# Kernel optimization log

Hardware: AMD Instinct MI355X
Metric: run time of the kernel (lower is better)

Reference implementation:

```python
import jax, jax.numpy as jnp
import numpy as np

N = 100000
E = 1600000
IN_FEATS = 512
N_HIDDEN = 128
N_CLASSES = 40


def setup_inputs() -> dict:
    key = jax.random.key(0)
    k1, k2, k3, k4, k5, k6, k7 = jax.random.split(key, 7)
    inputs = jax.random.normal(k1, (N, IN_FEATS), dtype=jnp.float32)
    edge_index = jax.random.randint(k2, (2, E), 0, N, dtype=jnp.int64)
    edge_attr = jax.random.uniform(k3, (E,), dtype=jnp.float32)
    # GCNConv params (Glorot-ish scaling)
    W1 = jax.random.normal(k4, (IN_FEATS, N_HIDDEN), dtype=jnp.float32) / np.sqrt(IN_FEATS)
    b1 = jnp.zeros((N_HIDDEN,), dtype=jnp.float32)
    W2 = jax.random.normal(k5, (N_HIDDEN, N_CLASSES), dtype=jnp.float32) / np.sqrt(N_HIDDEN)
    b2 = jnp.zeros((N_CLASSES,), dtype=jnp.float32)
    return {"inputs": inputs, "edge_index": edge_index, "edge_attr": edge_attr,
            "W1": W1, "b1": b1, "W2": W2, "b2": b2}


def gcn_conv(x, W, b, src, dst, edge_weight):
    """GCNConv with normalize=False: linear transform, then edge-weighted
    scatter-sum from src to dst, then bias."""
    m = x @ W                                   # [N, F_out]
    msgs = m[src] * edge_weight[:, None]        # gather + weight, [E, F_out]
    agg = jax.ops.segment_sum(msgs, dst, num_segments=x.shape[0])  # scatter-add
    return agg + b


def reference(inputs, edge_index, edge_attr, W1, b1, W2, b2):
    src, dst = edge_index[0], edge_index[1]
    h = jax.nn.relu(gcn_conv(inputs, W1, b1, src, dst, edge_attr))
    # F.dropout with training=False (eval mode) is identity -> deterministic baseline
    preds = gcn_conv(h, W2, b2, src, dst, edge_attr)
    return jax.nn.log_softmax(preds, axis=1)
```

## Files before the change

kernel.cpp:

```cpp
#include <hip/hip_runtime.h>
#include <hip/hip_bf16.h>
#include <cstdint>

#define N_NODES 100000
#define N_EDGES 1600000
#define F_IN    512
#define F_HID   128
#define F_OUT   40
#define F_OUT_PAD 48

#define BSH    8
#define NB     391
#define BEPT   8
#define BCHUNK 4096
#define GB     391
#define CONVB  140
#define FCAP   6144
#define DBINS  64

typedef short v8s __attribute__((ext_vector_type(8)));
typedef float v4f __attribute__((ext_vector_type(4)));

__device__ __forceinline__ short f2bf(float f) {
    unsigned u = __float_as_uint(f);
    u += 0x7fffu + ((u >> 16) & 1u);
    return (short)(u >> 16);
}

__device__ __forceinline__ float bflo(unsigned u) { return __uint_as_float(u << 16); }
__device__ __forceinline__ float bfhi(unsigned u) { return __uint_as_float(u & 0xffff0000u); }

__device__ __forceinline__ v8s pack8(float4 a, float4 b) {
    v8s r;
    r[0] = f2bf(a.x); r[1] = f2bf(a.y); r[2] = f2bf(a.z); r[3] = f2bf(a.w);
    r[4] = f2bf(b.x); r[5] = f2bf(b.y); r[6] = f2bf(b.z); r[7] = f2bf(b.w);
    return r;
}

__device__ __forceinline__ void gload16(const void* g, void* l) {
    __builtin_amdgcn_global_load_lds(
        (const __attribute__((address_space(1))) void*)g,
        (__attribute__((address_space(3))) void*)l, 16, 0, 0);
}


__global__ __launch_bounds__(512) void k_bhist(const int* __restrict__ dst,
                                               int* __restrict__ bcnt,
                                               const float* __restrict__ W1,
                                               short* __restrict__ WT1,
                                               const float* __restrict__ W2,
                                               short* __restrict__ WT2) {
    if (blockIdx.x >= GB) {
        int i = (blockIdx.x - GB) * 512 + threadIdx.x;
        if (i < F_IN * F_HID) {
            int n = i >> 9, k = i & 511;
            WT1[i] = f2bf(W1[k * F_HID + n]);
        } else {
            int j = i - F_IN * F_HID;
            if (j < F_OUT_PAD * F_HID) {
                int n = j >> 7, k = j & 127;
                WT2[j] = (n < F_OUT) ? f2bf(W2[k * F_OUT + n]) : (short)0;
            }
        }
        return;
    }
    __shared__ int lh[512];
    int tid = threadIdx.x;
    lh[tid] = 0;
    __syncthreads();
    long e0 = (long)blockIdx.x * BCHUNK;
#pragma unroll
    for (int i = 0; i < BEPT; i++) {
        long e = e0 + tid + i * 512;
        if (e < N_EDGES) atomicAdd(&lh[dst[e] >> BSH], 1);
    }
    __syncthreads();
    if (tid < NB && lh[tid]) atomicAdd(&bcnt[tid], lh[tid]);
}

__global__ __launch_bounds__(512) void k_bscan(const int* __restrict__ bcnt,
                                               int* __restrict__ bbase,
                                               int* __restrict__ bcur) {
    __shared__ int sm[512];
    int tid = threadIdx.x;
    int v = (tid < NB) ? bcnt[tid] : 0;
    sm[tid] = v;
    __syncthreads();
    for (int off = 1; off < 512; off <<= 1) {
        int t = (tid >= off) ? sm[tid - off] : 0;
        __syncthreads();
        sm[tid] += t;
        __syncthreads();
    }
    if (tid < NB) {
        int ex = sm[tid] - v;
        bbase[tid] = ex;
        bcur[tid] = ex;
    }
    if (tid == 511) bbase[NB] = sm[511];
}

__global__ __launch_bounds__(512) void k_bscatter(const int* __restrict__ src,
                                                  const int* __restrict__ dst,
                                                  const float* __restrict__ w,
                                                  int* __restrict__ bcur,
                                                  int2* __restrict__ tmp) {
    __shared__ int cntA[512];
    __shared__ int ofsA[512];
    __shared__ int lcur[512];
    __shared__ int gb[512];
    __shared__ __align__(16) int2 recBuf[BCHUNK];
    __shared__ unsigned short bkt[BCHUNK];
    int tid = threadIdx.x;
    long e0 = (long)blockIdx.x * BCHUNK;
    cntA[tid] = 0;
    __syncthreads();

    int dloc[BEPT];
#pragma unroll
    for (int i = 0; i < BEPT; i++) {
        long e = e0 + tid + i * 512;
        int d = (e < N_EDGES) ? dst[e] : -1;
        dloc[i] = d;
        if (d >= 0) atomicAdd(&cntA[d >> BSH], 1);
    }
    __syncthreads();

    int v = cntA[tid];
    ofsA[tid] = v;
    __syncthreads();
    for (int off = 1; off < 512; off <<= 1) {
        int t = (tid >= off) ? ofsA[tid - off] : 0;
        __syncthreads();
        ofsA[tid] += t;
        __syncthreads();
    }
    int excl = ofsA[tid] - v;
    ofsA[tid] = excl;
    lcur[tid] = excl;
    if (tid < NB && v > 0) gb[tid] = atomicAdd(&bcur[tid], v);
    __syncthreads();

#pragma unroll
    for (int i = 0; i < BEPT; i++) {
        int d = dloc[i];
        if (d >= 0) {
            long e = e0 + tid + i * 512;
            int j = d >> BSH;
            int slot = atomicAdd(&lcur[j], 1);
            recBuf[slot] = make_int2(src[e] | ((d & 255) << 17), __float_as_int(w[e]));
            bkt[slot] = (unsigned short)j;
        }
    }
    __syncthreads();

    long rem = N_EDGES - e0;
    int total = (rem < BCHUNK) ? (int)rem : BCHUNK;
    for (int s = tid; s < total; s += 512) {
        int j = bkt[s];
        tmp[gb[j] + (s - ofsA[j])] = recBuf[s];
    }
}

__global__ __launch_bounds__(256) void k_fine(const int2* __restrict__ tmp,
                                              const int* __restrict__ bbase,
                                              int2* __restrict__ rec,
                                              int* __restrict__ rowptr,
                                              int* __restrict__ deg,
                                              int* __restrict__ dcnt) {
    __shared__ int hist[256];
    __shared__ int ofs[256];
    __shared__ int cur[256];
    __shared__ int dh[DBINS];
    __shared__ __align__(16) int2 recOut[FCAP];
    int tid = threadIdx.x, b = blockIdx.x;
    int base = bbase[b];
    int cnt = bbase[b + 1] - base;

    hist[tid] = 0;
    if (tid < DBINS) dh[tid] = 0;
    __syncthreads();
    for (int i = tid; i < cnt; i += 256) {
        unsigned u = (unsigned)tmp[base + i].x;
        atomicAdd(&hist[u >> 17], 1);
    }
    __syncthreads();

    int v = hist[tid];
    ofs[tid] = v;
    __syncthreads();
    for (int off = 1; off < 256; off <<= 1) {
        int t = (tid >= off) ? ofs[tid - off] : 0;
        __syncthreads();
        ofs[tid] += t;
        __syncthreads();
    }
    int excl = ofs[tid] - v;
    ofs[tid] = excl;
    cur[tid] = excl;
    int node = (b << BSH) + tid;
    if (node < N_NODES) {
        rowptr[node] = base + excl;
        deg[node] = v;
        atomicAdd(&dh[v < DBINS ? v : DBINS - 1], 1);
    }
    __syncthreads();
    if (tid < DBINS && dh[tid]) atomicAdd(&dcnt[tid], dh[tid]);

    if (cnt <= FCAP) {
        for (int i = tid; i < cnt; i += 256) {
            int2 r = tmp[base + i];
            unsigned u = (unsigned)r.x;
            int slot = atomicAdd(&cur[u >> 17], 1);
            recOut[slot] = make_int2((int)(u & 0x1FFFFu), r.y);
        }
        __syncthreads();
        for (int i = tid; i < cnt; i += 256) rec[base + i] = recOut[i];
    } else {
        for (int i = tid; i < cnt; i += 256) {
            int2 r = tmp[base + i];
            unsigned u = (unsigned)r.x;
            int slot = atomicAdd(&cur[u >> 17], 1);
            rec[base + slot] = make_int2((int)(u & 0x1FFFFu), r.y);
        }
    }
}

__global__ __launch_bounds__(DBINS) void k_dscan(const int* __restrict__ dcnt,
                                                 int* __restrict__ dcur) {
    __shared__ int sm[DBINS];
    int tid = threadIdx.x;
    int v = dcnt[tid];
    sm[tid] = v;
    __syncthreads();
    for (int off = 1; off < DBINS; off <<= 1) {
        int t = (tid >= off) ? sm[tid - off] : 0;
        __syncthreads();
        sm[tid] += t;
        __syncthreads();
    }
    dcur[tid] = sm[tid] - v;
}

__global__ __launch_bounds__(256) void k_dscatter(const int* __restrict__ rowptr,
                                                  const int* __restrict__ deg,
                                                  int* __restrict__ dcur,
                                                  int4* __restrict__ ninfo) {
    __shared__ int lh[DBINS];
    __shared__ int gbase[DBINS];
    int tid = threadIdx.x;
    if (tid < DBINS) lh[tid] = 0;
    __syncthreads();
    int node = blockIdx.x * 256 + tid;
    int d = 0, lpos = 0, st = 0, ct = 0;
    bool valid = node < N_NODES;
    if (valid) {
        st = rowptr[node];
        ct = deg[node];
        d = ct < DBINS ? ct : DBINS - 1;
        lpos = atomicAdd(&lh[d], 1);
    }
    __syncthreads();
    if (tid < DBINS && lh[tid]) gbase[tid] = atomicAdd(&dcur[tid], lh[tid]);
    __syncthreads();
    if (valid) ninfo[gbase[d] + lpos] = make_int4(node, st, ct, 0);
}


__global__ __launch_bounds__(256) void k_gemm1(const float* __restrict__ x,
                                               const short* __restrict__ WT1,
                                               unsigned short* __restrict__ m1b) {
    __shared__ __align__(16) float aBuf[2][64 * 32];
    __shared__ __align__(16) short bBuf[2][128 * 32];
    int tid = threadIdx.x, w = tid >> 6, lane = tid & 63;
    int quad = lane >> 4, l16 = lane & 15;
    long rowBase = (long)blockIdx.x * 64;

    int ar = lane >> 3, ac = lane & 7;
    int br = lane >> 2, bc = lane & 3;

    v4f acc[8];
#pragma unroll
    for (int t = 0; t < 8; t++) acc[t] = (v4f){0.f, 0.f, 0.f, 0.f};

    auto stage = [&](int kc, int buf) {
#pragma unroll
        for (int i = 0; i < 2; i++) {
            int rl = w * 16 + i * 8 + ar;
            long rg = rowBase + rl;
            if (rg > N_NODES - 1) rg = N_NODES - 1;
            const float* gp = x + rg * F_IN + kc * 32 + ((ac ^ (rl & 7)) << 2);
            gload16(gp, &aBuf[buf][(w * 16 + i * 8) * 32]);
        }
#pragma unroll
        for (int i = 0; i < 2; i++) {
            int n = w * 32 + i * 16 + br;
            const short* gp = WT1 + n * F_IN + kc * 32 + ((bc ^ ((n >> 1) & 3)) << 3);
            gload16(gp, &bBuf[buf][(w * 32 + i * 16) * 32]);
        }
    };

    stage(0, 0);
#pragma unroll
    for (int kc = 0; kc < 16; kc++) {
        __syncthreads();
        int buf = kc & 1;
        if (kc < 15) stage(kc + 1, buf ^ 1);
        int arow = w * 16 + l16;
        int p0 = (2 * quad) ^ (l16 & 7);
        float4 av0 = *(const float4*)&aBuf[buf][arow * 32 + p0 * 4];
        float4 av1 = *(const float4*)&aBuf[buf][arow * 32 + (p0 ^ 1) * 4];
        v8s af = pack8(av0, av1);
#pragma unroll
        for (int t = 0; t < 8; t++) {
            int n = t * 16 + l16;
            int p = quad ^ ((n >> 1) & 3);
            v8s bf = *(const v8s*)&bBuf[buf][n * 32 + p * 8];
            acc[t] = __builtin_amdgcn_mfma_f32_16x16x32_bf16(af, bf, acc[t], 0, 0, 0);
        }
    }

#pragma unroll
    for (int t = 0; t < 8; t++)
#pragma unroll
        for (int r = 0; r < 4; r++) {
            long row = rowBase + w * 16 + quad * 4 + r;
            if (row < N_NODES)
                m1b[row * F_HID + t * 16 + l16] = (unsigned short)f2bf(acc[t][r]);
        }
}


__global__ void k_agg1(const int2* __restrict__ rec, const int4* __restrict__ ninfo,
                       const uint4* __restrict__ m1v, const float* __restrict__ b1,
                       uint4* __restrict__ h4) {
    int gid = blockIdx.x * 4 + (threadIdx.x >> 6);
    int lane = threadIdx.x & 63;
    if (gid >= N_NODES) return;
    int4 ni = ninfo[gid];
    int node = ni.x, start = ni.y, cnt = ni.z;
    int q = lane >> 4, l16 = lane & 15;

    float a0 = 0.f, a1 = 0.f, a2 = 0.f, a3 = 0.f;
    float a4 = 0.f, a5 = 0.f, a6 = 0.f, a7 = 0.f;
    float c0 = 0.f, c1 = 0.f, c2 = 0.f, c3 = 0.f;
    float c4 = 0.f, c5 = 0.f, c6 = 0.f, c7 = 0.f;

    int nmain = cnt >> 3;
    int eb = start + q;
    for (int k = 0; k < nmain; k++) {
        int e = eb + (k << 3);
        int2 r0 = rec[e];
        int2 r1 = rec[e + 4];
        uint4 g0 = m1v[(long)r0.x * 16 + l16];
        uint4 g1 = m1v[(long)r1.x * 16 + l16];
        float w0 = __int_as_float(r0.y), w1 = __int_as_float(r1.y);
        a0 = fmaf(w0, bflo(g0.x), a0); a1 = fmaf(w0, bfhi(g0.x), a1);
        a2 = fmaf(w0, bflo(g0.y), a2); a3 = fmaf(w0, bfhi(g0.y), a3);
        a4 = fmaf(w0, bflo(g0.z), a4); a5 = fmaf(w0, bfhi(g0.z), a5);
        a6 = fmaf(w0, bflo(g0.w), a6); a7 = fmaf(w0, bfhi(g0.w), a7);
        c0 = fmaf(w1, bflo(g1.x), c0); c1 = fmaf(w1, bfhi(g1.x), c1);
        c2 = fmaf(w1, bflo(g1.y), c2); c3 = fmaf(w1, bfhi(g1.y), c3);
        c4 = fmaf(w1, bflo(g1.z), c4); c5 = fmaf(w1, bfhi(g1.z), c5);
        c6 = fmaf(w1, bflo(g1.w), c6); c7 = fmaf(w1, bfhi(g1.w), c7);
    }
    for (int e = start + (nmain << 3) + q; e < start + cnt; e += 4) {
        int2 r = rec[e];
        uint4 g = m1v[(long)r.x * 16 + l16];
        float w = __int_as_float(r.y);
        a0 = fmaf(w, bflo(g.x), a0); a1 = fmaf(w, bfhi(g.x), a1);
        a2 = fmaf(w, bflo(g.y), a2); a3 = fmaf(w, bfhi(g.y), a3);
        a4 = fmaf(w, bflo(g.z), a4); a5 = fmaf(w, bfhi(g.z), a5);
        a6 = fmaf(w, bflo(g.w), a6); a7 = fmaf(w, bfhi(g.w), a7);
    }
    a0 += c0; a1 += c1; a2 += c2; a3 += c3;
    a4 += c4; a5 += c5; a6 += c6; a7 += c7;
    a0 += __shfl_xor(a0, 16); a0 += __shfl_xor(a0, 32);
    a1 += __shfl_xor(a1, 16); a1 += __shfl_xor(a1, 32);
    a2 += __shfl_xor(a2, 16); a2 += __shfl_xor(a2, 32);
    a3 += __shfl_xor(a3, 16); a3 += __shfl_xor(a3, 32);
    a4 += __shfl_xor(a4, 16); a4 += __shfl_xor(a4, 32);
    a5 += __shfl_xor(a5, 16); a5 += __shfl_xor(a5, 32);
    a6 += __shfl_xor(a6, 16); a6 += __shfl_xor(a6, 32);
    a7 += __shfl_xor(a7, 16); a7 += __shfl_xor(a7, 32);
    if (q == 0) {
        const float4* b4 = (const float4*)b1;
        float4 bv0 = b4[2 * l16], bv1 = b4[2 * l16 + 1];
        a0 = fmaxf(a0 + bv0.x, 0.f); a1 = fmaxf(a1 + bv0.y, 0.f);
        a2 = fmaxf(a2 + bv0.z, 0.f); a3 = fmaxf(a3 + bv0.w, 0.f);
        a4 = fmaxf(a4 + bv1.x, 0.f); a5 = fmaxf(a5 + bv1.y, 0.f);
        a6 = fmaxf(a6 + bv1.z, 0.f); a7 = fmaxf(a7 + bv1.w, 0.f);
        uint4 o;
        o.x = (unsigned)(unsigned short)f2bf(a0) | ((unsigned)(unsigned short)f2bf(a1) << 16);
        o.y = (unsigned)(unsigned short)f2bf(a2) | ((unsigned)(unsigned short)f2bf(a3) << 16);
        o.z = (unsigned)(unsigned short)f2bf(a4) | ((unsigned)(unsigned short)f2bf(a5) << 16);
        o.w = (unsigned)(unsigned short)f2bf(a6) | ((unsigned)(unsigned short)f2bf(a7) << 16);
        h4[(long)node * 16 + l16] = o;
    }
}


__global__ __launch_bounds__(256) void k_gemm2(const unsigned short* __restrict__ h,
                                               const short* __restrict__ WT2,
                                               unsigned short* __restrict__ m2b) {
    int wave = threadIdx.x >> 6, lane = threadIdx.x & 63;
    int quad = lane >> 4, l16 = lane & 15;
    long rowBase = ((long)blockIdx.x * 4 + wave) * 16;
    if (rowBase >= N_NODES) return;

    v4f acc[3];
#pragma unroll
    for (int t = 0; t < 3; t++) acc[t] = (v4f){0.f, 0.f, 0.f, 0.f};

    const short* arow = (const short*)h + (rowBase + l16) * (long)F_HID + quad * 8;
    const short* brow = WT2 + l16 * F_HID + quad * 8;
#pragma unroll
    for (int k0 = 0; k0 < F_HID; k0 += 32) {
        v8s af = *reinterpret_cast<const v8s*>(arow + k0);
#pragma unroll
        for (int t = 0; t < 3; t++) {
            v8s bf = *reinterpret_cast<const v8s*>(brow + t * 16 * F_HID + k0);
            acc[t] = __builtin_amdgcn_mfma_f32_16x16x32_bf16(af, bf, acc[t], 0, 0, 0);
        }
    }
#pragma unroll
    for (int r = 0; r < 4; r++) {
        long row = rowBase + quad * 4 + r;
#pragma unroll
        for (int t = 0; t < 3; t++)
            m2b[row * 64 + t * 16 + l16] = (unsigned short)f2bf(acc[t][r]);
        m2b[row * 64 + 48 + l16] = 0;
    }
}


__global__ void k_agg2(const int2* __restrict__ rec, const int4* __restrict__ ninfo,
                       const uint4* __restrict__ m2v, const float* __restrict__ b2,
                       float* __restrict__ out) {
    int gid = blockIdx.x * 4 + (threadIdx.x >> 6);
    int lane = threadIdx.x & 63;
    if (gid >= N_NODES) return;
    int4 ni = ninfo[gid];
    int node = ni.x, start = ni.y, cnt = ni.z;
    int oc = lane >> 3, l8 = lane & 7;

    float a0 = 0.f, a1 = 0.f, a2 = 0.f, a3 = 0.f;
    float a4 = 0.f, a5 = 0.f, a6 = 0.f, a7 = 0.f;

    int nmain = cnt >> 3;
    int eb = start + oc;
    for (int k = 0; k < nmain; k++) {
        int2 r = rec[eb + (k << 3)];
        uint4 g = m2v[(long)r.x * 8 + l8];
        float w = __int_as_float(r.y);
        a0 = fmaf(w, bflo(g.x), a0); a1 = fmaf(w, bfhi(g.x), a1);
        a2 = fmaf(w, bflo(g.y), a2); a3 = fmaf(w, bfhi(g.y), a3);
        a4 = fmaf(w, bflo(g.z), a4); a5 = fmaf(w, bfhi(g.z), a5);
        a6 = fmaf(w, bflo(g.w), a6); a7 = fmaf(w, bfhi(g.w), a7);
    }
    {
        int e = start + (nmain << 3) + oc;
        if (e < start + cnt) {
            int2 r = rec[e];
            uint4 g = m2v[(long)r.x * 8 + l8];
            float w = __int_as_float(r.y);
            a0 = fmaf(w, bflo(g.x), a0); a1 = fmaf(w, bfhi(g.x), a1);
            a2 = fmaf(w, bflo(g.y), a2); a3 = fmaf(w, bfhi(g.y), a3);
            a4 = fmaf(w, bflo(g.z), a4); a5 = fmaf(w, bfhi(g.z), a5);
            a6 = fmaf(w, bflo(g.w), a6); a7 = fmaf(w, bfhi(g.w), a7);
        }
    }
#pragma unroll
    for (int off = 8; off < 64; off <<= 1) {
        a0 += __shfl_xor(a0, off); a1 += __shfl_xor(a1, off);
        a2 += __shfl_xor(a2, off); a3 += __shfl_xor(a3, off);
        a4 += __shfl_xor(a4, off); a5 += __shfl_xor(a5, off);
        a6 += __shfl_xor(a6, off); a7 += __shfl_xor(a7, off);
    }

    const float NEG = -3.4e38f;
    float v0 = NEG, v1 = NEG, v2 = NEG, v3 = NEG;
    float v4 = NEG, v5 = NEG, v6 = NEG, v7 = NEG;
    if (l8 < 5) {
        const float4* b4 = (const float4*)b2;
        float4 bv0 = b4[2 * l8], bv1 = b4[2 * l8 + 1];
        v0 = a0 + bv0.x; v1 = a1 + bv0.y; v2 = a2 + bv0.z; v3 = a3 + bv0.w;
        v4 = a4 + bv1.x; v5 = a5 + bv1.y; v6 = a6 + bv1.z; v7 = a7 + bv1.w;
    }
    float m = fmaxf(fmaxf(fmaxf(v0, v1), fmaxf(v2, v3)),
                    fmaxf(fmaxf(v4, v5), fmaxf(v6, v7)));
#pragma unroll
    for (int off = 1; off < 8; off <<= 1) m = fmaxf(m, __shfl_xor(m, off));
    float s = 0.f;
    if (l8 < 5)
        s = __expf(v0 - m) + __expf(v1 - m) + __expf(v2 - m) + __expf(v3 - m) +
            __expf(v4 - m) + __expf(v5 - m) + __expf(v6 - m) + __expf(v7 - m);
#pragma unroll
    for (int off = 1; off < 8; off <<= 1) s += __shfl_xor(s, off);
    if (oc == 0 && l8 < 5) {
        float ls = m + __logf(s);
        float4* op = (float4*)(out + (long)node * F_OUT);
        float4 o0, o1;
        o0.x = v0 - ls; o0.y = v1 - ls; o0.z = v2 - ls; o0.w = v3 - ls;
        o1.x = v4 - ls; o1.y = v5 - ls; o1.z = v6 - ls; o1.w = v7 - ls;
        op[2 * l8] = o0;
        op[2 * l8 + 1] = o1;
    }
}


extern "C" void kernel_launch(void* const* d_in, const int* in_sizes, int n_in,
                              void* d_out, int out_size, void* d_ws, size_t ws_size,
                              hipStream_t stream) {
    const float* x  = (const float*)d_in[0];
    const int* ei   = (const int*)d_in[1];
    const int* src  = ei;
    const int* dst  = ei + N_EDGES;
    const float* ew = (const float*)d_in[2];
    const float* W1 = (const float*)d_in[3];
    const float* b1 = (const float*)d_in[4];
    const float* W2 = (const float*)d_in[5];
    const float* b2 = (const float*)d_in[6];
    float* out = (float*)d_out;

    char* ws = (char*)d_ws;
    size_t off = 0;
    auto alloc = [&](size_t bytes) {
        void* p = ws + off;
        off += (bytes + 255) & ~(size_t)255;
        return p;
    };
    unsigned short* m1b  = (unsigned short*)alloc((size_t)N_NODES * F_HID * 2);
    unsigned int*   h    = (unsigned int*)alloc((size_t)N_NODES * F_HID * 2);
    unsigned short* m2b  = (unsigned short*)alloc((size_t)N_NODES * 64 * 2);
    int2*           rec  = (int2*)alloc((size_t)N_EDGES * 8);
    int*          rowptr = (int*)alloc((size_t)N_NODES * 4);
    int*          deg    = (int*)alloc((size_t)N_NODES * 4);
    int4*         ninfo  = (int4*)alloc((size_t)N_NODES * 16);
    int*          ctrl   = (int*)alloc(1024 * 4);
    int*          bBase  = (int*)alloc(512 * 4);
    int*          bCur   = (int*)alloc(512 * 4);
    short*        WT1    = (short*)alloc((size_t)F_HID * F_IN * 2);
    short*        WT2    = (short*)alloc((size_t)F_OUT_PAD * F_HID * 2);

    int* bCnt = ctrl;
    int* dcnt = ctrl + 512;
    int* dcur = ctrl + 576;

    int2* tmp = (int2*)m2b;

    hipMemsetAsync(ctrl, 0, 576 * 4, stream);

    k_bhist<<<GB + CONVB, 512, 0, stream>>>(dst, bCnt, W1, WT1, W2, WT2);
    k_bscan<<<1, 512, 0, stream>>>(bCnt, bBase, bCur);
    k_bscatter<<<GB, 512, 0, stream>>>(src, dst, ew, bCur, tmp);
    k_fine<<<NB, 256, 0, stream>>>(tmp, bBase, rec, rowptr, deg, dcnt);
    k_dscan<<<1, DBINS, 0, stream>>>(dcnt, dcur);
    k_dscatter<<<(N_NODES + 255) / 256, 256, 0, stream>>>(rowptr, deg, dcur, ninfo);

    k_gemm1<<<(N_NODES + 63) / 64, 256, 0, stream>>>(x, WT1, m1b);
    k_agg1<<<(N_NODES + 3) / 4, 256, 0, stream>>>(rec, ninfo, (const uint4*)m1b,
                                                  b1, (uint4*)h);
    k_gemm2<<<(N_NODES + 63) / 64, 256, 0, stream>>>((const unsigned short*)h, WT2, m2b);
    k_agg2<<<(N_NODES + 3) / 4, 256, 0, stream>>>(rec, ninfo, (const uint4*)m2b,
                                                  b2, out);
}
```

Measured before the change: 502.9 us.

## Fuse layer-1 aggregation with second GEMM and drop degree-sorted node ordering

Removes the degree-bucketing pipeline (histogram, scan and scatter kernels plus ninfo) and iterates nodes in natural order using rowptr/deg directly. Layer-1 aggregation now processes 16 consecutive nodes per wave, stages the bf16 hidden rows in swizzled LDS, and applies the W2 MFMA in-register, so the hidden matrix h never goes to global memory and k_gemm2 is eliminated. The edge loops are unrolled 4-way in the first layer and 2-way in the second. In exchange, removing degree sorting can cause load imbalance across waves, and each wave handles its 16 nodes serially.

Measured after the change: 491.0 us. 2.4% less time.

```diff
diff --git a/kernel.cpp b/kernel.cpp
--- a/kernel.cpp
+++ b/kernel.cpp
@@ -16,7 +16,6 @@
 #define GB     391
 #define CONVB  140
 #define FCAP   6144
-#define DBINS  64
 
 typedef short v8s __attribute__((ext_vector_type(8)));
 typedef float v4f __attribute__((ext_vector_type(4)));
@@ -166,19 +165,16 @@
                                               const int* __restrict__ bbase,
                                               int2* __restrict__ rec,
                                               int* __restrict__ rowptr,
-                                              int* __restrict__ deg,
-                                              int* __restrict__ dcnt) {
+                                              int* __restrict__ deg) {
     __shared__ int hist[256];
     __shared__ int ofs[256];
     __shared__ int cur[256];
-    __shared__ int dh[DBINS];
     __shared__ __align__(16) int2 recOut[FCAP];
     int tid = threadIdx.x, b = blockIdx.x;
     int base = bbase[b];
     int cnt = bbase[b + 1] - base;
 
     hist[tid] = 0;
-    if (tid < DBINS) dh[tid] = 0;
     __syncthreads();
     for (int i = tid; i < cnt; i += 256) {
         unsigned u = (unsigned)tmp[base + i].x;
@@ -202,10 +198,8 @@
     if (node < N_NODES) {
         rowptr[node] = base + excl;
         deg[node] = v;
-        atomicAdd(&dh[v < DBINS ? v : DBINS - 1], 1);
-    }
-    __syncthreads();
-    if (tid < DBINS && dh[tid]) atomicAdd(&dcnt[tid], dh[tid]);
+    }
+    __syncthreads();
 
     if (cnt <= FCAP) {
         for (int i = tid; i < cnt; i += 256) {
@@ -224,46 +218,6 @@
             rec[base + slot] = make_int2((int)(u & 0x1FFFFu), r.y);
         }
     }
-}
-
-__global__ __launch_bounds__(DBINS) void k_dscan(const int* __restrict__ dcnt,
-                                                 int* __restrict__ dcur) {
-    __shared__ int sm[DBINS];
-    int tid = threadIdx.x;
-    int v = dcnt[tid];
-    sm[tid] = v;
-    __syncthreads();
-    for (int off = 1; off < DBINS; off <<= 1) {
-        int t = (tid >= off) ? sm[tid - off] : 0;
-        __syncthreads();
-        sm[tid] += t;
-        __syncthreads();
-    }
-    dcur[tid] = sm[tid] - v;
-}
-
-__global__ __launch_bounds__(256) void k_dscatter(const int* __restrict__ rowptr,
-                                                  const int* __restrict__ deg,
-                                                  int* __restrict__ dcur,
-                                                  int4* __restrict__ ninfo) {
-    __shared__ int lh[DBINS];
-    __shared__ int gbase[DBINS];
-    int tid = threadIdx.x;
-    if (tid < DBINS) lh[tid] = 0;
-    __syncthreads();
-    int node = blockIdx.x * 256 + tid;
-    int d = 0, lpos = 0, st = 0, ct = 0;
-    bool valid = node < N_NODES;
-    if (valid) {
-        st = rowptr[node];
-        ct = deg[node];
-        d = ct < DBINS ? ct : DBINS - 1;
-        lpos = atomicAdd(&lh[d], 1);
-    }
-    __syncthreads();
-    if (tid < DBINS && lh[tid]) gbase[tid] = atomicAdd(&dcur[tid], lh[tid]);
-    __syncthreads();
-    if (valid) ninfo[gbase[d] + lpos] = make_int4(node, st, ct, 0);
 }
 
 
@@ -331,144 +285,182 @@
 }
 
 
-__global__ void k_agg1(const int2* __restrict__ rec, const int4* __restrict__ ninfo,
-                       const uint4* __restrict__ m1v, const float* __restrict__ b1,
-                       uint4* __restrict__ h4) {
-    int gid = blockIdx.x * 4 + (threadIdx.x >> 6);
+__global__ __launch_bounds__(256) void k_ag(const int2* __restrict__ rec,
+                                            const int* __restrict__ rowptr,
+                                            const int* __restrict__ deg,
+                                            const uint4* __restrict__ m1v,
+                                            const float* __restrict__ b1,
+                                            const short* __restrict__ WT2,
+                                            unsigned short* __restrict__ m2b) {
+    __shared__ uint4 ht[4][16][16];
+    int tid = threadIdx.x, w = tid >> 6, lane = tid & 63;
+    int q = lane >> 4, l16 = lane & 15;
+    int gBase = (blockIdx.x * 4 + w) * 16;
+
+    int idx = gBase + l16;
+    int rp = 0, dg = 0;
+    if (idx < N_NODES) { rp = rowptr[idx]; dg = deg[idx]; }
+    const float4* b4 = (const float4*)b1;
+    float4 bv0 = b4[2 * l16], bv1 = b4[2 * l16 + 1];
+
+    for (int i = 0; i < 16; i++) {
+        int start = __shfl(rp, i);
+        int cnt = __shfl(dg, i);
+        float a0 = 0.f, a1 = 0.f, a2 = 0.f, a3 = 0.f;
+        float a4 = 0.f, a5 = 0.f, a6 = 0.f, a7 = 0.f;
+        int e = start + q;
+        int n16 = cnt >> 4;
+        for (int k = 0; k < n16; k++) {
+            int2 r0 = rec[e];
+            int2 r1 = rec[e + 4];
+            int2 r2 = rec[e + 8];
+            int2 r3 = rec[e + 12];
+            uint4 g0 = m1v[(long)r0.x * 16 + l16];
+            uint4 g1 = m1v[(long)r1.x * 16 + l16];
+            uint4 g2 = m1v[(long)r2.x * 16 + l16];
+            uint4 g3 = m1v[(long)r3.x * 16 + l16];
+            float w0 = __int_as_float(r0.y), w1 = __int_as_float(r1.y);
+            float w2 = __int_as_float(r2.y), w3 = __int_as_float(r3.y);
+            a0 = fmaf(w0, bflo(g0.x), a0); a1 = fmaf(w0, bfhi(g0.x), a1);
+            a2 = fmaf(w0, bflo(g0.y), a2); a3 = fmaf(w0, bfhi(g0.y), a3);
+            a4 = fmaf(w0, bflo(g0.z), a4); a5 = fmaf(w0, bfhi(g0.z), a5);
+            a6 = fmaf(w0, bflo(g0.w), a6); a7 = fmaf(w0, bfhi(g0.w), a7);
+            a0 = fmaf(w1, bflo(g1.x), a0); a1 = fmaf(w1, bfhi(g1.x), a1);
+            a2 = fmaf(w1, bflo(g1.y), a2); a3 = fmaf(w1, bfhi(g1.y), a3);
+            a4 = fmaf(w1, bflo(g1.z), a4); a5 = fmaf(w1, bfhi(g1.z), a5);
+            a6 = fmaf(w1, bflo(g1.w), a6); a7 = fmaf(w1, bfhi(g1.w), a7);
+            a0 = fmaf(w2, bflo(g2.x), a0); a1 = fmaf(w2, bfhi(g2.x), a1);
+            a2 = fmaf(w2, bflo(g2.y), a2); a3 = fmaf(w2, bfhi(g2.y), a3);
+            a4 = fmaf(w2, bflo(g2.z), a4); a5 = fmaf(w2, bfhi(g2.z), a5);
+            a6 = fmaf(w2, bflo(g2.w), a6); a7 = fmaf(w2, bfhi(g2.w), a7);
+            a0 = fmaf(w3, bflo(g3.x), a0); a1 = fmaf(w3, bfhi(g3.x), a1);
+            a2 = fmaf(w3, bflo(g3.y), a2); a3 = fmaf(w3, bfhi(g3.y), a3);
+            a4 = fmaf(w3, bflo(g3.z), a4); a5 = fmaf(w3, bfhi(g3.z), a5);
+            a6 = fmaf(w3, bflo(g3.w), a6); a7 = fmaf(w3, bfhi(g3.w), a7);
+            e += 16;
+        }
+        if (cnt & 8) {
+            int2 r0 = rec[e];
+            int2 r1 = rec[e + 4];
+            uint4 g0 = m1v[(long)r0.x * 16 + l16];
+            uint4 g1 = m1v[(long)r1.x * 16 + l16];
+            float w0 = __int_as_float(r0.y), w1 = __int_as_float(r1.y);
+            a0 = fmaf(w0, bflo(g0.x), a0); a1 = fmaf(w0, bfhi(g0.x), a1);
+            a2 = fmaf(w0, bflo(g0.y), a2); a3 = fmaf(w0, bfhi(g0.y), a3);
+            a4 = fmaf(w0, bflo(g0.z), a4); a5 = fmaf(w0, bfhi(g0.z), a5);
+            a6 = fmaf(w0, bflo(g0.w), a6); a7 = fmaf(w0, bfhi(g0.w), a7);
+            a0 = fmaf(w1, bflo(g1.x), a0); a1 = fmaf(w1, bfhi(g1.x), a1);
+            a2 = fmaf(w1, bflo(g1.y), a2); a3 = fmaf(w1, bfhi(g1.y), a3);
+            a4 = fmaf(w1, bflo(g1.z), a4); a5 = fmaf(w1, bfhi(g1.z), a5);
+            a6 = fmaf(w1, bflo(g1.w), a6); a7 = fmaf(w1, bfhi(g1.w), a7);
+            e += 8;
+        }
+        for (int t = e; t < start + cnt; t += 4) {
+            int2 r = rec[t];
+            uint4 g = m1v[(long)r.x * 16 + l16];
+            float ww = __int_as_float(r.y);
+            a0 = fmaf(ww, bflo(g.x), a0); a1 = fmaf(ww, bfhi(g.x), a1);
+            a2 = fmaf(ww, bflo(g.y), a2); a3 = fmaf(ww, bfhi(g.y), a3);
+            a4 = fmaf(ww, bflo(g.z), a4); a5 = fmaf(ww, bfhi(g.z), a5);
+            a6 = fmaf(ww, bflo(g.w), a6); a7 = fmaf(ww, bfhi(g.w), a7);
+        }
+        a0 += __shfl_xor(a0, 16); a0 += __shfl_xor(a0, 32);
+        a1 += __shfl_xor(a1, 16); a1 += __shfl_xor(a1, 32);
+        a2 += __shfl_xor(a2, 16); a2 += __shfl_xor(a2, 32);
+        a3 += __shfl_xor(a3, 16); a3 += __shfl_xor(a3, 32);
+        a4 += __shfl_xor(a4, 16); a4 += __shfl_xor(a4, 32);
+        a5 += __shfl_xor(a5, 16); a5 += __shfl_xor(a5, 32);
+        a6 += __shfl_xor(a6, 16); a6 += __shfl_xor(a6, 32);
+        a7 += __shfl_xor(a7, 16); a7 += __shfl_xor(a7, 32);
+        if (q == 0) {
+            a0 = fmaxf(a0 + bv0.x, 0.f); a1 = fmaxf(a1 + bv0.y, 0.f);
+            a2 = fmaxf(a2 + bv0.z, 0.f); a3 = fmaxf(a3 + bv0.w, 0.f);
+            a4 = fmaxf(a4 + bv1.x, 0.f); a5 = fmaxf(a5 + bv1.y, 0.f);
+            a6 = fmaxf(a6 + bv1.z, 0.f); a7 = fmaxf(a7 + bv1.w, 0.f);
+            uint4 o;
+            o.x = (unsigned)(unsigned short)f2bf(a0) | ((unsigned)(unsigned short)f2bf(a1) << 16);
+            o.y = (unsigned)(unsigned short)f2bf(a2) | ((unsigned)(unsigned short)f2bf(a3) << 16);
+            o.z = (unsigned)(unsigned short)f2bf(a4) | ((unsigned)(unsigned short)f2bf(a5) << 16);
+            o.w = (unsigned)(unsigned short)f2bf(a6) | ((unsigned)(unsigned short)f2bf(a7) << 16);
+            ht[w][i][l16 ^ (i & 7)] = o;
+        }
+    }
+
+    v4f acc[3];
+#pragma unroll
+    for (int t = 0; t < 3; t++) acc[t] = (v4f){0.f, 0.f, 0.f, 0.f};
+#pragma unroll
+    for (int kk = 0; kk < 4; kk++) {
+        uint4 av = ht[w][l16][(kk * 4 + q) ^ (l16 & 7)];
+        v8s af = *reinterpret_cast<const v8s*>(&av);
+        const short* brow = WT2 + l16 * F_HID + q * 8 + kk * 32;
+#pragma unroll
+        for (int t = 0; t < 3; t++) {
+            v8s bf = *reinterpret_cast<const v8s*>(brow + t * 16 * F_HID);
+            acc[t] = __builtin_amdgcn_mfma_f32_16x16x32_bf16(af, bf, acc[t], 0, 0, 0);
+        }
+    }
+#pragma unroll
+    for (int r = 0; r < 4; r++) {
+        int g = gBase + q * 4 + r;
+        if (g < N_NODES) {
+#pragma unroll
+            for (int t = 0; t < 3; t++)
+                m2b[(long)g * 64 + t * 16 + l16] = (unsigned short)f2bf(acc[t][r]);
+            m2b[(long)g * 64 + 48 + l16] = 0;
+        }
+    }
+}
+
+
+__global__ void k_agg2(const int2* __restrict__ rec, const int* __restrict__ rowptr,
+                       const int* __restrict__ deg, const uint4* __restrict__ m2v,
+                       const float* __restrict__ b2, float* __restrict__ out) {
+    int node = blockIdx.x * 4 + (threadIdx.x >> 6);
     int lane = threadIdx.x & 63;
-    if (gid >= N_NODES) return;
-    int4 ni = ninfo[gid];
-    int node = ni.x, start = ni.y, cnt = ni.z;
-    int q = lane >> 4, l16 = lane & 15;
+    if (node >= N_NODES) return;
+    int start = rowptr[node], cnt = deg[node];
+    int oc = lane >> 3, l8 = lane & 7;
 
     float a0 = 0.f, a1 = 0.f, a2 = 0.f, a3 = 0.f;
     float a4 = 0.f, a5 = 0.f, a6 = 0.f, a7 = 0.f;
-    float c0 = 0.f, c1 = 0.f, c2 = 0.f, c3 = 0.f;
-    float c4 = 0.f, c5 = 0.f, c6 = 0.f, c7 = 0.f;
-
-    int nmain = cnt >> 3;
-    int eb = start + q;
-    for (int k = 0; k < nmain; k++) {
-        int e = eb + (k << 3);
+
+    int e = start + oc;
+    int n16 = cnt >> 4;
+    for (int k = 0; k < n16; k++) {
         int2 r0 = rec[e];
-        int2 r1 = rec[e + 4];
-        uint4 g0 = m1v[(long)r0.x * 16 + l16];
-        uint4 g1 = m1v[(long)r1.x * 16 + l16];
+        int2 r1 = rec[e + 8];
+        uint4 g0 = m2v[(long)r0.x * 8 + l8];
+        uint4 g1 = m2v[(long)r1.x * 8 + l8];
         float w0 = __int_as_float(r0.y), w1 = __int_as_float(r1.y);
         a0 = fmaf(w0, bflo(g0.x), a0); a1 = fmaf(w0, bfhi(g0.x), a1);
         a2 = fmaf(w0, bflo(g0.y), a2); a3 = fmaf(w0, bfhi(g0.y), a3);
         a4 = fmaf(w0, bflo(g0.z), a4); a5 = fmaf(w0, bfhi(g0.z), a5);
         a6 = fmaf(w0, bflo(g0.w), a6); a7 = fmaf(w0, bfhi(g0.w), a7);
-        c0 = fmaf(w1, bflo(g1.x), c0); c1 = fmaf(w1, bfhi(g1.x), c1);
-        c2 = fmaf(w1, bflo(g1.y), c2); c3 = fmaf(w1, bfhi(g1.y), c3);
-        c4 = fmaf(w1, bflo(g1.z), c4); c5 = fmaf(w1, bfhi(g1.z), c5);
-        c6 = fmaf(w1, bflo(g1.w), c6); c7 = fmaf(w1, bfhi(g1.w), c7);
-    }
-    for (int e = start + (nmain << 3) + q; e < start + cnt; e += 4) {
+        a0 = fmaf(w1, bflo(g1.x), a0); a1 = fmaf(w1, bfhi(g1.x), a1);
+        a2 = fmaf(w1, bflo(g1.y), a2); a3 = fmaf(w1, bfhi(g1.y), a3);
+        a4 = fmaf(w1, bflo(g1.z), a4); a5 = fmaf(w1, bfhi(g1.z), a5);
+        a6 = fmaf(w1, bflo(g1.w), a6); a7 = fmaf(w1, bfhi(g1.w), a7);
+        e += 16;
+    }
+    if (cnt & 8) {
         int2 r = rec[e];
-        uint4 g = m1v[(long)r.x * 16 + l16];
-        float w = __int_as_float(r.y);
-        a0 = fmaf(w, bflo(g.x), a0); a1 = fmaf(w, bfhi(g.x), a1);
-        a2 = fmaf(w, bflo(g.y), a2); a3 = fmaf(w, bfhi(g.y), a3);
-        a4 = fmaf(w, bflo(g.z), a4); a5 = fmaf(w, bfhi(g.z), a5);
-        a6 = fmaf(w, bflo(g.w), a6); a7 = fmaf(w, bfhi(g.w), a7);
-    }
-    a0 += c0; a1 += c1; a2 += c2; a3 += c3;
-    a4 += c4; a5 += c5; a6 += c6; a7 += c7;
-    a0 += __shfl_xor(a0, 16); a0 += __shfl_xor(a0, 32);
-    a1 += __shfl_xor(a1, 16); a1 += __shfl_xor(a1, 32);
-    a2 += __shfl_xor(a2, 16); a2 += __shfl_xor(a2, 32);
-    a3 += __shfl_xor(a3, 16); a3 += __shfl_xor(a3, 32);
-    a4 += __shfl_xor(a4, 16); a4 += __shfl_xor(a4, 32);
-    a5 += __shfl_xor(a5, 16); a5 += __shfl_xor(a5, 32);
-    a6 += __shfl_xor(a6, 16); a6 += __shfl_xor(a6, 32);
-    a7 += __shfl_xor(a7, 16); a7 += __shfl_xor(a7, 32);
-    if (q == 0) {
-        const float4* b4 = (const float4*)b1;
-        float4 bv0 = b4[2 * l16], bv1 = b4[2 * l16 + 1];
-        a0 = fmaxf(a0 + bv0.x, 0.f); a1 = fmaxf(a1 + bv0.y, 0.f);
-        a2 = fmaxf(a2 + bv0.z, 0.f); a3 = fmaxf(a3 + bv0.w, 0.f);
-        a4 = fmaxf(a4 + bv1.x, 0.f); a5 = fmaxf(a5 + bv1.y, 0.f);
-        a6 = fmaxf(a6 + bv1.z, 0.f); a7 = fmaxf(a7 + bv1.w, 0.f);
-        uint4 o;
-        o.x = (unsigned)(unsigned short)f2bf(a0) | ((unsigned)(unsigned short)f2bf(a1) << 16);
-        o.y = (unsigned)(unsigned short)f2bf(a2) | ((unsigned)(unsigned short)f2bf(a3) << 16);
-        o.z = (unsigned)(unsigned short)f2bf(a4) | ((unsigned)(unsigned short)f2bf(a5) << 16);
-        o.w = (unsigned)(unsigned short)f2bf(a6) | ((unsigned)(unsigned short)f2bf(a7) << 16);
-        h4[(long)node * 16 + l16] = o;
-    }
-}
-
-
-__global__ __launch_bounds__(256) void k_gemm2(const unsigned short* __restrict__ h,
-                                               const short* __restrict__ WT2,
-                                               unsigned short* __restrict__ m2b) {
-    int wave = threadIdx.x >> 6, lane = threadIdx.x & 63;
-    int quad = lane >> 4, l16 = lane & 15;
-    long rowBase = ((long)blockIdx.x * 4 + wave) * 16;
-    if (rowBase >= N_NODES) return;
-
-    v4f acc[3];
-#pragma unroll
-    for (int t = 0; t < 3; t++) acc[t] = (v4f){0.f, 0.f, 0.f, 0.f};
-
-    const short* arow = (const short*)h + (rowBase + l16) * (long)F_HID + quad * 8;
-    const short* brow = WT2 + l16 * F_HID + quad * 8;
-#pragma unroll
-    for (int k0 = 0; k0 < F_HID; k0 += 32) {
-        v8s af = *reinterpret_cast<const v8s*>(arow + k0);
-#pragma unroll
-        for (int t = 0; t < 3; t++) {
-            v8s bf = *reinterpret_cast<const v8s*>(brow + t * 16 * F_HID + k0);
-            acc[t] = __builtin_amdgcn_mfma_f32_16x16x32_bf16(af, bf, acc[t], 0, 0, 0);
-        }
-    }
-#pragma unroll
-    for (int r = 0; r < 4; r++) {
-        long row = rowBase + quad * 4 + r;
-#pragma unroll
-        for (int t = 0; t < 3; t++)
-            m2b[row * 64 + t * 16 + l16] = (unsigned short)f2bf(acc[t][r]);
-        m2b[row * 64 + 48 + l16] = 0;
-    }
-}
-
-
-__global__ void k_agg2(const int2* __restrict__ rec, const int4* __restrict__ ninfo,
-                       const uint4* __restrict__ m2v, const float* __restrict__ b2,
-                       float* __restrict__ out) {
-    int gid = blockIdx.x * 4 + (threadIdx.x >> 6);
-    int lane = threadIdx.x & 63;
-    if (gid >= N_NODES) return;
-    int4 ni = ninfo[gid];
-    int node = ni.x, start = ni.y, cnt = ni.z;
-    int oc = lane >> 3, l8 = lane & 7;
-
-    float a0 = 0.f, a1 = 0.f, a2 = 0.f, a3 = 0.f;
-    float a4 = 0.f, a5 = 0.f, a6 = 0.f, a7 = 0.f;
-
-    int nmain = cnt >> 3;
-    int eb = start + oc;
-    for (int k = 0; k < nmain; k++) {
-        int2 r = rec[eb + (k << 3)];
         uint4 g = m2v[(long)r.x * 8 + l8];
         float w = __int_as_float(r.y);
         a0 = fmaf(w, bflo(g.x), a0); a1 = fmaf(w, bfhi(g.x), a1);
         a2 = fmaf(w, bflo(g.y), a2); a3 = fmaf(w, bfhi(g.y), a3);
         a4 = fmaf(w, bflo(g.z), a4); a5 = fmaf(w, bfhi(g.z), a5);
         a6 = fmaf(w, bflo(g.w), a6); a7 = fmaf(w, bfhi(g.w), a7);
-    }
-    {
-        int e = start + (nmain << 3) + oc;
-        if (e < start + cnt) {
-            int2 r = rec[e];
-            uint4 g = m2v[(long)r.x * 8 + l8];
-            float w = __int_as_float(r.y);
-            a0 = fmaf(w, bflo(g.x), a0); a1 = fmaf(w, bfhi(g.x), a1);
-            a2 = fmaf(w, bflo(g.y), a2); a3 = fmaf(w, bfhi(g.y), a3);
-            a4 = fmaf(w, bflo(g.z), a4); a5 = fmaf(w, bfhi(g.z), a5);
-            a6 = fmaf(w, bflo(g.w), a6); a7 = fmaf(w, bfhi(g.w), a7);
-        }
+        e += 8;
+    }
+    if (e < start + cnt) {
+        int2 r = rec[e];
+        uint4 g = m2v[(long)r.x * 8 + l8];
+        float w = __int_as_float(r.y);
+        a0 = fmaf(w, bflo(g.x), a0); a1 = fmaf(w, bfhi(g.x), a1);
+        a2 = fmaf(w, bflo(g.y), a2); a3 = fmaf(w, bfhi(g.y), a3);
+        a4 = fmaf(w, bflo(g.z), a4); a5 = fmaf(w, bfhi(g.z), a5);
+        a6 = fmaf(w, bflo(g.w), a6); a7 = fmaf(w, bfhi(g.w), a7);
     }
 #pragma unroll
     for (int off = 8; off < 64; off <<= 1) {
@@ -531,37 +523,28 @@
         return p;
     };
     unsigned short* m1b  = (unsigned short*)alloc((size_t)N_NODES * F_HID * 2);
-    unsigned int*   h    = (unsigned int*)alloc((size_t)N_NODES * F_HID * 2);
     unsigned short* m2b  = (unsigned short*)alloc((size_t)N_NODES * 64 * 2);
     int2*           rec  = (int2*)alloc((size_t)N_EDGES * 8);
     int*          rowptr = (int*)alloc((size_t)N_NODES * 4);
     int*          deg    = (int*)alloc((size_t)N_NODES * 4);
-    int4*         ninfo  = (int4*)alloc((size_t)N_NODES * 16);
-    int*          ctrl   = (int*)alloc(1024 * 4);
+    int*          bCnt   = (int*)alloc(512 * 4);
     int*          bBase  = (int*)alloc(512 * 4);
     int*          bCur   = (int*)alloc(512 * 4);
     short*        WT1    = (short*)alloc((size_t)F_HID * F_IN * 2);
     short*        WT2    = (short*)alloc((size_t)F_OUT_PAD * F_HID * 2);
 
-    int* bCnt = ctrl;
-    int* dcnt = ctrl + 512;
-    int* dcur = ctrl + 576;
-
     int2* tmp = (int2*)m2b;
 
-    hipMemsetAsync(ctrl, 0, 576 * 4, stream);
+    hipMemsetAsync(bCnt, 0, 512 * 4, stream);
 
     k_bhist<<<GB + CONVB, 512, 0, stream>>>(dst, bCnt, W1, WT1, W2, WT2);
     k_bscan<<<1, 512, 0, stream>>>(bCnt, bBase, bCur);
     k_bscatter<<<GB, 512, 0, stream>>>(src, dst, ew, bCur, tmp);
-    k_fine<<<NB, 256, 0, stream>>>(tmp, bBase, rec, rowptr, deg, dcnt);
-    k_dscan<<<1, DBINS, 0, stream>>>(dcnt, dcur);
-    k_dscatter<<<(N_NODES + 255) / 256, 256, 0, stream>>>(rowptr, deg, dcur, ninfo);
+    k_fine<<<NB, 256, 0, stream>>>(tmp, bBase, rec, rowptr, deg);
 
     k_gemm1<<<(N_NODES + 63) / 64, 256, 0, stream>>>(x, WT1, m1b);
-    k_agg1<<<(N_NODES + 3) / 4, 256, 0, stream>>>(rec, ninfo, (const uint4*)m1b,
-                                                  b1, (uint4*)h);
-    k_gemm2<<<(N_NODES + 63) / 64, 256, 0, stream>>>((const unsigned short*)h, WT2, m2b);
-    k_agg2<<<(N_NODES + 3) / 4, 256, 0, stream>>>(rec, ninfo, (const uint4*)m2b,
-                                                  b2, out);
-}
+    k_ag<<<(N_NODES + 63) / 64, 256, 0, stream>>>(rec, rowptr, deg,
+                                                  (const uint4*)m1b, b1, WT2, m2b);
+    k_agg2<<<(N_NODES + 3) / 4, 256, 0, stream>>>(rec, rowptr, deg,
+                                                  (const uint4*)m2b, b2, out);
+}
```
